# Kernel tuning notes

Hardware: AMD Instinct MI355X
Metric: run time of the kernel (lower is better)

## Reference

```python
import jax, jax.numpy as jnp
import numpy as np

DIM = 2048
HID = 1024
E = 16
TOP_K = 2
S_SHARED = 2


def setup_inputs() -> dict:
    key = jax.random.key(0)
    ks = jax.random.split(key, 6)
    scale = 0.02
    x = jax.random.normal(ks[0], (2, 2048, DIM), dtype=jnp.float32)
    gate_w = jax.random.normal(ks[1], (DIM, E), dtype=jnp.float32) * scale
    shared_w1 = jax.random.normal(ks[2], (S_SHARED, DIM, HID), dtype=jnp.float32) * scale
    shared_w2 = jax.random.normal(ks[3], (S_SHARED, HID, DIM), dtype=jnp.float32) * scale
    w1 = jax.random.normal(ks[4], (E, DIM, HID), dtype=jnp.float32) * scale
    w2 = jax.random.normal(ks[5], (E, HID, DIM), dtype=jnp.float32) * scale
    return {"x": x, "gate_w": gate_w, "shared_w1": shared_w1,
            "shared_w2": shared_w2, "w1": w1, "w2": w2}


def reference(x, gate_w, shared_w1, shared_w2, w1, w2):
    orig_shape = x.shape
    xf = x.reshape(-1, orig_shape[-1])  # [T, D]

    # Shared experts: sum of SiLU MLPs
    hs = jax.nn.silu(jnp.einsum('td,sdh->sth', xf, shared_w1))
    shared_out = jnp.einsum('sth,shd->td', hs, shared_w2)

    # Gating
    probs = jax.nn.softmax(xf @ gate_w, axis=-1)              # [T, E]
    weights, indices = jax.lax.top_k(probs, TOP_K)            # [T, K]
    weights = weights / weights.sum(axis=-1, keepdims=True)
    aux_loss = (probs.mean(axis=0) ** 2).sum() * E

    # Combine weights per (token, expert): top_k indices are distinct
    combine = (jax.nn.one_hot(indices, E, dtype=xf.dtype) *
               weights[..., None]).sum(axis=1)                # [T, E]

    # Dense all-expert compute (reference form of gather-GEMM-scatter)
    h = jax.nn.silu(jnp.einsum('td,edh->eth', xf, w1))        # [E, T, H]
    y = jnp.einsum('eth,ehd->etd', h, w2)                     # [E, T, D]
    routed_out = jnp.einsum('te,etd->td', combine, y)         # [T, D]

    out = (shared_out + routed_out).reshape(orig_shape)
    return out, aux_loss
```

## Files before the change

### kernel.cpp

```cpp
#include <hip/hip_runtime.h>
#include <math.h>

typedef unsigned short u16;
typedef __bf16 bf16x8 __attribute__((ext_vector_type(8)));
typedef float f32x4 __attribute__((ext_vector_type(4)));
typedef unsigned short u16x8 __attribute__((ext_vector_type(8)));

#define T_TOK 4096
#define DIMD 2048
#define HIDD 1024
#define NEXP 16
#define RMAX 10240
#define MAXBLK 96
#define BM 128
#define BN 256
#define BK 64

__device__ __forceinline__ u16 f2b(float f) {
  unsigned u = __builtin_bit_cast(unsigned, f);
  unsigned r = (u + 0x7FFFu + ((u >> 16) & 1u)) >> 16;
  return (u16)r;
}

__device__ __forceinline__ void gld16(const void* g, void* l) {
  __builtin_amdgcn_global_load_lds(
      (const __attribute__((address_space(1))) void*)g,
      (__attribute__((address_space(3))) void*)l, 16, 0, 0);
}


__global__ void k_pre(const float* __restrict__ x, u16* __restrict__ xb,
                      int* __restrict__ perm, int* __restrict__ cnt) {
  const int i = blockIdx.x * blockDim.x + threadIdx.x;
  const float4 v = ((const float4*)x)[i];
  union { u16 u[4]; unsigned long long q; } t;
  t.u[0] = f2b(v.x); t.u[1] = f2b(v.y); t.u[2] = f2b(v.z); t.u[3] = f2b(v.w);
  ((unsigned long long*)xb)[i] = t.q;
  if (i < RMAX) perm[i] = -1;
  if (i < NEXP) cnt[i] = 0;
}

__global__ __launch_bounds__(256)
void k_gate(const float* __restrict__ x, const float* __restrict__ gw,
            int* __restrict__ top2i, float* __restrict__ top2w,
            int* __restrict__ cnt, float* __restrict__ partial) {
  const int e = threadIdx.x & 15;
  const int tt = threadIdx.x >> 4;
  const int t = blockIdx.x * 16 + tt;
  const float* xp = x + (size_t)t * DIMD;
  float acc = 0.f;
#pragma unroll 8
  for (int k = 0; k < DIMD; ++k) acc = fmaf(xp[k], gw[k * NEXP + e], acc);
  __shared__ float lg[16][17];
  __shared__ float pr[16][17];
  lg[tt][e] = acc;
  __syncthreads();
  if (e == 0) {
    float l[16];
    float mx = -1e30f;
    for (int j = 0; j < 16; ++j) { l[j] = lg[tt][j]; mx = fmaxf(mx, l[j]); }
    float s = 0.f;
    for (int j = 0; j < 16; ++j) { l[j] = expf(l[j] - mx); s += l[j]; }
    const float inv = 1.f / s;
    float p1 = -1.f, p2 = -1.f; int i1 = 0, i2 = 0;
    for (int j = 0; j < 16; ++j) {
      const float p = l[j] * inv;
      pr[tt][j] = p;
      if (p > p1) { p2 = p1; i2 = i1; p1 = p; i1 = j; }
      else if (p > p2) { p2 = p; i2 = j; }
    }
    const float wsum = p1 + p2;
    top2i[t * 2 + 0] = i1;
    top2i[t * 2 + 1] = i2;
    top2w[t * 2 + 0] = p1 / wsum;
    top2w[t * 2 + 1] = p2 / wsum;
    atomicAdd(&cnt[i1], 1);
    atomicAdd(&cnt[i2], 1);
  }
  __syncthreads();
  if (tt == 0) {
    float s = 0.f;
    for (int j = 0; j < 16; ++j) s += pr[j][e];
    partial[blockIdx.x * 16 + e] = s;
  }
}

__global__ __launch_bounds__(256)
void k_sched(const int* __restrict__ cnt, const int* __restrict__ top2i,
             const float* __restrict__ top2w, const float* __restrict__ partial,
             int* __restrict__ tbl_e, int* __restrict__ tbl_r0,
             int* __restrict__ nblk, int* __restrict__ perm,
             float* __restrict__ wrow, int* __restrict__ slot2,
             float* __restrict__ auxOut) {
  __shared__ int offs[17];
  __shared__ int lfill[16];
  __shared__ float s[16][17];
  const int tid = threadIdx.x;
  if (tid == 0) {
    int o = 0, nb = 0;
    for (int e = 0; e < NEXP; ++e) {
      offs[e] = o;
      const int b = (cnt[e] + BM - 1) / BM;
      for (int i = 0; i < b; ++i) { tbl_e[nb] = e; tbl_r0[nb] = o + i * BM; ++nb; }
      o += b * BM;
    }
    offs[16] = o;
    nblk[0] = nb;
  }
  if (tid < 16) lfill[tid] = 0;
  __syncthreads();
  for (int id = tid; id < T_TOK * 2; id += 256) {
    const int e = top2i[id];
    const int pos = atomicAdd(&lfill[e], 1);
    const int r = offs[e] + pos;
    perm[r] = id >> 1;
    wrow[r] = top2w[id];
    slot2[id] = r;
  }
  const int e = tid & 15, c = tid >> 4;
  float a = 0.f;
  for (int b = c; b < 256; b += 16) a += partial[b * 16 + e];
  s[c][e] = a;
  __syncthreads();
  if (tid == 0) {
    float aux = 0.f;
    for (int j = 0; j < 16; ++j) {
      float tot = 0.f;
      for (int cc = 0; cc < 16; ++cc) tot += s[cc][j];
      const float m = tot / (float)T_TOK;
      aux += m * m;
    }
    auxOut[0] = aux * (float)NEXP;
  }
}

__global__ __launch_bounds__(256)
void k_trW(const float* __restrict__ w1, const float* __restrict__ w2,
           const float* __restrict__ sw1, const float* __restrict__ sw2,
           u16* __restrict__ w1t, u16* __restrict__ w2t,
           u16* __restrict__ sw1t, u16* __restrict__ sw2ct) {
  const int z = blockIdx.z;
  const float* W; u16* Wo; int K, N, ldo;
  if (z < 16) {
    W = w1 + (size_t)z * 2048 * 1024;
    Wo = w1t + (size_t)z * 1024 * 2048;
    K = 2048; N = 1024; ldo = 2048;
  } else if (z < 32) {
    W = w2 + (size_t)(z - 16) * 1024 * 2048;
    Wo = w2t + (size_t)(z - 16) * 2048 * 1024;
    K = 1024; N = 2048; ldo = 1024;
  } else if (z < 34) {
    W = sw1 + (size_t)(z - 32) * 2048 * 1024;
    Wo = sw1t + (size_t)(z - 32) * 1024 * 2048;
    K = 2048; N = 1024; ldo = 2048;
  } else {
    W = sw2 + (size_t)(z - 34) * 1024 * 2048;
    Wo = sw2ct + (size_t)(z - 34) * 1024;
    K = 1024; N = 2048; ldo = 2048;
  }
  const int n0 = blockIdx.x * 64, k0 = blockIdx.y * 64;
  if (n0 >= N || k0 >= K) return;
  __shared__ float t[64][65];
  {
    const int r = threadIdx.x >> 4;
    const int c = (threadIdx.x & 15) * 4;
#pragma unroll
    for (int p = 0; p < 4; ++p) {
      const int kk = p * 16 + r;
      const float4 v = *(const float4*)&W[(size_t)(k0 + kk) * N + n0 + c];
      t[kk][c] = v.x; t[kk][c + 1] = v.y; t[kk][c + 2] = v.z; t[kk][c + 3] = v.w;
    }
  }
  __syncthreads();
  {
    const int r2 = threadIdx.x >> 3;
    const int g8 = (threadIdx.x & 7) * 8;
#pragma unroll
    for (int p = 0; p < 2; ++p) {
      const int nn = p * 32 + r2;
      u16x8 o;
#pragma unroll
      for (int i = 0; i < 8; ++i) o[i] = f2b(t[g8 + i][nn]);
      *(u16x8*)&Wo[(size_t)(n0 + nn) * ldo + k0 + g8] = o;
    }
  }
}

__global__ __launch_bounds__(512)
void k_post(float* __restrict__ out, const float* __restrict__ rbLo,
            const float* __restrict__ rbHi, const int* __restrict__ slot2,
            const float* __restrict__ wrow) {
  const int t = blockIdx.x;
  const int d4 = threadIdx.x;
  const int s0 = slot2[t * 2], s1 = slot2[t * 2 + 1];
  const float w0 = wrow[s0], w1 = wrow[s1];
  const float4* r0 = (const float4*)(s0 < 8192 ? rbLo + (size_t)s0 * DIMD
                                               : rbHi + (size_t)(s0 - 8192) * DIMD);
  const float4* r1 = (const float4*)(s1 < 8192 ? rbLo + (size_t)s1 * DIMD
                                               : rbHi + (size_t)(s1 - 8192) * DIMD);
  float4* op = (float4*)(out + (size_t)t * DIMD);
  float4 o = op[d4];
  const float4 a = r0[d4], b = r1[d4];
  o.x += w0 * a.x + w1 * b.x;
  o.y += w0 * a.y + w1 * b.y;
  o.z += w0 * a.z + w1 * b.z;
  o.w += w0 * a.w + w1 * b.w;
  op[d4] = o;
}


__device__ __forceinline__ void stage_tile(
    const u16* gA0, const u16* gA1, const u16* gB0, const u16* gB1,
    const u16* gB2, const u16* gB3, int k0, u16* S, int b, int w) {
  u16* As = S + b * 24576;
  u16* Bs = As + 8192;
  gld16(gA0 + k0, As + w * 512);
  gld16(gA1 + k0, As + 4096 + w * 512);
  gld16(gB0 + k0, Bs + w * 512);
  gld16(gB1 + k0, Bs + 4096 + w * 512);
  gld16(gB2 + k0, Bs + 8192 + w * 512);
  gld16(gB3 + k0, Bs + 12288 + w * 512);
}

__device__ __forceinline__ void comp_tile(const u16* __restrict__ S, int b,
    const int (&aoff)[4][2], const int (&boff)[4][2], f32x4 (&acc)[4][4]) {
  const u16* As = S + b * 24576;
  const u16* Bs = As + 8192;
#pragma unroll
  for (int kh = 0; kh < 2; ++kh) {
    bf16x8 a[4], bq[4];
#pragma unroll
    for (int i = 0; i < 4; ++i) a[i] = *(const bf16x8*)(As + aoff[i][kh]);
#pragma unroll
    for (int j = 0; j < 4; ++j) bq[j] = *(const bf16x8*)(Bs + boff[j][kh]);
    __builtin_amdgcn_s_setprio(1);
#pragma unroll
    for (int i = 0; i < 4; ++i)
#pragma unroll
      for (int j = 0; j < 4; ++j)
        acc[i][j] = __builtin_amdgcn_mfma_f32_16x16x32_bf16(a[i], bq[j], acc[i][j], 0, 0, 0);
    __builtin_amdgcn_s_setprio(0);
  }
}

#define FENCE asm volatile("" ::: "memory")
#define VMW6  asm volatile("s_waitcnt vmcnt(6)" ::: "memory")
#define VMW0  asm volatile("s_waitcnt vmcnt(0)" ::: "memory")

__device__ __forceinline__ void gemm_pipe(
    const u16* gA0, const u16* gA1, const u16* gB0, const u16* gB1,
    const u16* gB2, const u16* gB3, int K, u16* S,
    const int (&aoff)[4][2], const int (&boff)[4][2],
    f32x4 (&acc)[4][4], int w) {
  const int nt = K >> 6;
  stage_tile(gA0, gA1, gB0, gB1, gB2, gB3, 0, S, 0, w);
  stage_tile(gA0, gA1, gB0, gB1, gB2, gB3, 64, S, 1, w);
  VMW6;
  __builtin_amdgcn_s_barrier();
  FENCE;
  for (int t = 0; t < nt - 2; ++t) {
    comp_tile(S, t & 1, aoff, boff, acc);
    FENCE;
    __builtin_amdgcn_s_barrier();
    FENCE;
    stage_tile(gA0, gA1, gB0, gB1, gB2, gB3, (t + 2) << 6, S, t & 1, w);
    VMW6;
    __builtin_amdgcn_s_barrier();
    FENCE;
  }
  comp_tile(S, 0, aoff, boff, acc);
  VMW0;
  __builtin_amdgcn_s_barrier();
  FENCE;
  comp_tile(S, 1, aoff, boff, acc);
}

__global__ __launch_bounds__(512, 2)
void k_up(const u16* __restrict__ xb, const u16* __restrict__ sw1t,
          const u16* __restrict__ w1t, u16* __restrict__ hbS,
          u16* __restrict__ hbR, const int* __restrict__ perm,
          const int* __restrict__ tbl_e, const int* __restrict__ tbl_r0,
          const int* __restrict__ nblk) {
  __shared__ u16 S[49152];
  const int bx = blockIdx.x, by = blockIdx.y;
  const int tid = threadIdx.x;
  const int w = tid >> 6, lane = tid & 63;
  const int lm = lane & 15, lq = lane >> 4;
  const int wm = w >> 2, wn = w & 3;
  const int srow = w * 8 + (lane >> 3);
  const int c8 = lane & 7;

  const bool routed = bx >= 32;
  int r0, ga0, ga1;
  const u16* Bb;
  if (!routed) {
    r0 = bx * BM;
    Bb = sw1t;
    ga0 = r0 + srow; ga1 = r0 + 64 + srow;
  } else {
    if (by >= 4) return;
    const int rbx = bx - 32;
    if (rbx >= *nblk) return;
    const int e = tbl_e[rbx];
    r0 = tbl_r0[rbx];
    Bb = w1t + (size_t)e * (size_t)HIDD * DIMD;
    const int p0 = perm[r0 + srow];      ga0 = (p0 < 0) ? 0 : p0;
    const int p1 = perm[r0 + 64 + srow]; ga1 = (p1 < 0) ? 0 : p1;
  }
  const int n0 = by * BN;
  const u16* gA0 = xb + (size_t)ga0 * DIMD + (c8 ^ ((srow >> 1) & 7)) * 8;
  const u16* gA1 = xb + (size_t)ga1 * DIMD + (c8 ^ (((64 + srow) >> 1) & 7)) * 8;
  const u16* gB[4];
#pragma unroll
  for (int p = 0; p < 4; ++p) {
    const int n = p * 64 + srow;
    gB[p] = Bb + (size_t)(n0 + n) * DIMD + (c8 ^ ((n >> 1) & 7)) * 8;
  }
  int aoff[4][2], boff[4][2];
#pragma unroll
  for (int i = 0; i < 4; ++i) {
    const int m = wm * 64 + i * 16 + lm;
    const int n = wn * 64 + i * 16 + lm;
#pragma unroll
    for (int kh = 0; kh < 2; ++kh) {
      aoff[i][kh] = m * 64 + (((kh << 2) | lq) ^ ((m >> 1) & 7)) * 8;
      boff[i][kh] = n * 64 + (((kh << 2) | lq) ^ ((n >> 1) & 7)) * 8;
    }
  }
  f32x4 acc[4][4];
#pragma unroll
  for (int i = 0; i < 4; ++i)
#pragma unroll
    for (int j = 0; j < 4; ++j) {
      acc[i][j][0] = 0.f; acc[i][j][1] = 0.f; acc[i][j][2] = 0.f; acc[i][j][3] = 0.f;
    }

  gemm_pipe(gA0, gA1, gB[0], gB[1], gB[2], gB[3], DIMD, S, aoff, boff, acc, w);

#pragma unroll
  for (int i = 0; i < 4; ++i) {
#pragma unroll
    for (int r = 0; r < 4; ++r) {
      const int row = r0 + wm * 64 + i * 16 + lq * 4 + r;
      u16* dst = routed ? &hbR[(size_t)row * HIDD] : &hbS[(size_t)row * DIMD];
#pragma unroll
      for (int j = 0; j < 4; ++j) {
        const int gc = n0 + wn * 64 + j * 16 + lm;
        const float v = acc[i][j][r];
        const float s = v / (1.f + expf(-v));
        dst[gc] = f2b(s);
      }
    }
  }
}

__global__ __launch_bounds__(512, 2)
void k_down(const u16* __restrict__ hbS, const u16* __restrict__ hbR,
            const u16* __restrict__ sw2ct, const u16* __restrict__ w2t,
            float* __restrict__ out, float* __restrict__ rbLo,
            float* __restrict__ rbHi, const int* __restrict__ tbl_e,
            const int* __restrict__ tbl_r0, const int* __restrict__ nblk) {
  __shared__ u16 S[49152];
  const int bx = blockIdx.x, by = blockIdx.y;
  const int tid = threadIdx.x;
  const int w = tid >> 6, lane = tid & 63;
  const int lm = lane & 15, lq = lane >> 4;
  const int wm = w >> 2, wn = w & 3;
  const int srow = w * 8 + (lane >> 3);
  const int c8 = lane & 7;

  const bool routed = bx >= 32;
  int r0, K, ld;
  const u16 *Ab, *Bb;
  if (!routed) {
    r0 = bx * BM;
    Ab = hbS; K = DIMD; ld = DIMD;
    Bb = sw2ct;
  } else {
    const int rbx = bx - 32;
    if (rbx >= *nblk) return;
    const int e = tbl_e[rbx];
    r0 = tbl_r0[rbx];
    Ab = hbR; K = HIDD; ld = HIDD;
    Bb = w2t + (size_t)e * (size_t)DIMD * HIDD;
  }
  const int n0 = by * BN;
  const u16* gA0 = Ab + (size_t)(r0 + srow) * ld + (c8 ^ ((srow >> 1) & 7)) * 8;
  const u16* gA1 = Ab + (size_t)(r0 + 64 + srow) * ld + (c8 ^ (((64 + srow) >> 1) & 7)) * 8;
  const u16* gB[4];
#pragma unroll
  for (int p = 0; p < 4; ++p) {
    const int n = p * 64 + srow;
    gB[p] = Bb + (size_t)(n0 + n) * ld + (c8 ^ ((n >> 1) & 7)) * 8;
  }
  int aoff[4][2], boff[4][2];
#pragma unroll
  for (int i = 0; i < 4; ++i) {
    const int m = wm * 64 + i * 16 + lm;
    const int n = wn * 64 + i * 16 + lm;
#pragma unroll
    for (int kh = 0; kh < 2; ++kh) {
      aoff[i][kh] = m * 64 + (((kh << 2) | lq) ^ ((m >> 1) & 7)) * 8;
      boff[i][kh] = n * 64 + (((kh << 2) | lq) ^ ((n >> 1) & 7)) * 8;
    }
  }
  f32x4 acc[4][4];
#pragma unroll
  for (int i = 0; i < 4; ++i)
#pragma unroll
    for (int j = 0; j < 4; ++j) {
      acc[i][j][0] = 0.f; acc[i][j][1] = 0.f; acc[i][j][2] = 0.f; acc[i][j][3] = 0.f;
    }

  gemm_pipe(gA0, gA1, gB[0], gB[1], gB[2], gB[3], K, S, aoff, boff, acc, w);

#pragma unroll
  for (int i = 0; i < 4; ++i) {
#pragma unroll
    for (int r = 0; r < 4; ++r) {
      const int rr = r0 + wm * 64 + i * 16 + lq * 4 + r;
      float* dst;
      if (!routed) dst = out + (size_t)rr * DIMD;
      else dst = (rr < 8192) ? rbLo + (size_t)rr * DIMD
                             : rbHi + (size_t)(rr - 8192) * DIMD;
#pragma unroll
      for (int j = 0; j < 4; ++j) {
        const int gc = n0 + wn * 64 + j * 16 + lm;
        dst[gc] = acc[i][j][r];
      }
    }
  }
}


extern "C" void kernel_launch(void* const* d_in, const int* in_sizes, int n_in,
                              void* d_out, int out_size, void* d_ws, size_t ws_size,
                              hipStream_t stream) {
  const float* x   = (const float*)d_in[0];
  const float* gw  = (const float*)d_in[1];
  const float* sw1 = (const float*)d_in[2];
  const float* sw2 = (const float*)d_in[3];
  const float* w1  = (const float*)d_in[4];
  const float* w2  = (const float*)d_in[5];
  float* out = (float*)d_out;

  char* ws = (char*)d_ws;
  u16* xb    = (u16*)(ws);
  u16* hbS   = (u16*)(ws + (size_t)( 16 << 20));
  u16* hbR   = (u16*)(ws + (size_t)( 32 << 20));
  u16* sw1t  = (u16*)(ws + (size_t)( 56 << 20));
  u16* sw2ct = (u16*)(ws + (size_t)( 64 << 20));
  u16* w1t   = (u16*)(ws + (size_t)( 72 << 20));
  u16* w2t   = (u16*)(ws + (size_t)(136 << 20));
  float* rbLo = (float*)(ws + (size_t)( 72 << 20));
  float* rbHi = (float*)(ws);
  char* p = ws + (size_t)(200 << 20);
  int*   top2i   = (int*)p;    p += T_TOK * 2 * 4;
  float* top2w   = (float*)p;  p += T_TOK * 2 * 4;
  int*   perm    = (int*)p;    p += RMAX * 4;
  float* wrow    = (float*)p;  p += RMAX * 4;
  int*   slot2   = (int*)p;    p += T_TOK * 2 * 4;
  int*   cnt     = (int*)p;    p += 16 * 4;
  int*   tbl_e   = (int*)p;    p += MAXBLK * 4;
  int*   tbl_r0  = (int*)p;    p += MAXBLK * 4;
  int*   nblk    = (int*)p;    p += 16 * 4;
  float* partial = (float*)p;  p += 256 * 16 * 4;

  k_pre<<<(T_TOK * DIMD / 4) / 256, 256, 0, stream>>>(x, xb, perm, cnt);
  k_gate<<<T_TOK / 16, 256, 0, stream>>>(x, gw, top2i, top2w, cnt, partial);
  k_sched<<<1, 256, 0, stream>>>(cnt, top2i, top2w, partial, tbl_e, tbl_r0,
                                 nblk, perm, wrow, slot2,
                                 out + (size_t)T_TOK * DIMD);
  k_trW<<<dim3(32, 32, 36), 256, 0, stream>>>(w1, w2, sw1, sw2,
                                              w1t, w2t, sw1t, sw2ct);
  k_up<<<dim3(32 + MAXBLK, 8), 512, 0, stream>>>(xb, sw1t, w1t, hbS, hbR,
                                                 perm, tbl_e, tbl_r0, nblk);
  k_down<<<dim3(32 + MAXBLK, 8), 512, 0, stream>>>(hbS, hbR, sw2ct, w2t, out,
                                                   rbLo, rbHi, tbl_e, tbl_r0, nblk);
  k_post<<<T_TOK, 512, 0, stream>>>(out, rbLo, rbHi, slot2, wrow);
}
```

Measured before the change: 762.7 us.

## Enlarge GEMM tile to 256x256 with staggered LDS pipeline and token-ordered scatter

```diff
diff --git a/kernel.cpp b/kernel.cpp
--- a/kernel.cpp
+++ b/kernel.cpp
@@ -10,11 +10,10 @@
 #define DIMD 2048
 #define HIDD 1024
 #define NEXP 16
-#define RMAX 10240
-#define MAXBLK 96
-#define BM 128
+#define RMAX 12288
+#define MAXBLK 48
+#define BM 256
 #define BN 256
-#define BK 64
 
 __device__ __forceinline__ u16 f2b(float f) {
   unsigned u = __builtin_bit_cast(unsigned, f);
@@ -30,13 +29,14 @@
 
 
 __global__ void k_pre(const float* __restrict__ x, u16* __restrict__ xb,
-                      int* __restrict__ perm, int* __restrict__ cnt) {
+                      int* __restrict__ perm, int* __restrict__ perm2,
+                      int* __restrict__ cnt) {
   const int i = blockIdx.x * blockDim.x + threadIdx.x;
   const float4 v = ((const float4*)x)[i];
   union { u16 u[4]; unsigned long long q; } t;
   t.u[0] = f2b(v.x); t.u[1] = f2b(v.y); t.u[2] = f2b(v.z); t.u[3] = f2b(v.w);
   ((unsigned long long*)xb)[i] = t.q;
-  if (i < RMAX) perm[i] = -1;
+  if (i < RMAX) { perm[i] = -1; perm2[i] = -1; }
   if (i < NEXP) cnt[i] = 0;
 }
 
@@ -90,8 +90,7 @@
              const float* __restrict__ top2w, const float* __restrict__ partial,
              int* __restrict__ tbl_e, int* __restrict__ tbl_r0,
              int* __restrict__ nblk, int* __restrict__ perm,
-             float* __restrict__ wrow, int* __restrict__ slot2,
-             float* __restrict__ auxOut) {
+             int* __restrict__ perm2, float* __restrict__ auxOut) {
   __shared__ int offs[17];
   __shared__ int lfill[16];
   __shared__ float s[16][17];
@@ -114,8 +113,7 @@
     const int pos = atomicAdd(&lfill[e], 1);
     const int r = offs[e] + pos;
     perm[r] = id >> 1;
-    wrow[r] = top2w[id];
-    slot2[id] = r;
+    perm2[r] = id;
   }
   const int e = tid & 15, c = tid >> 4;
   float a = 0.f;
@@ -142,20 +140,16 @@
   const int z = blockIdx.z;
   const float* W; u16* Wo; int K, N, ldo;
   if (z < 16) {
-    W = w1 + (size_t)z * 2048 * 1024;
-    Wo = w1t + (size_t)z * 1024 * 2048;
+    W = w1 + (size_t)z * 2048 * 1024;  Wo = w1t + (size_t)z * 1024 * 2048;
     K = 2048; N = 1024; ldo = 2048;
   } else if (z < 32) {
-    W = w2 + (size_t)(z - 16) * 1024 * 2048;
-    Wo = w2t + (size_t)(z - 16) * 2048 * 1024;
+    W = w2 + (size_t)(z - 16) * 1024 * 2048;  Wo = w2t + (size_t)(z - 16) * 2048 * 1024;
     K = 1024; N = 2048; ldo = 1024;
   } else if (z < 34) {
-    W = sw1 + (size_t)(z - 32) * 2048 * 1024;
-    Wo = sw1t + (size_t)(z - 32) * 1024 * 2048;
+    W = sw1 + (size_t)(z - 32) * 2048 * 1024;  Wo = sw1t + (size_t)(z - 32) * 1024 * 2048;
     K = 2048; N = 1024; ldo = 2048;
   } else {
-    W = sw2 + (size_t)(z - 34) * 1024 * 2048;
-    Wo = sw2ct + (size_t)(z - 34) * 1024;
+    W = sw2 + (size_t)(z - 34) * 1024 * 2048;  Wo = sw2ct + (size_t)(z - 34) * 1024;
     K = 1024; N = 2048; ldo = 2048;
   }
   const int n0 = blockIdx.x * 64, k0 = blockIdx.y * 64;
@@ -187,20 +181,15 @@
 }
 
 __global__ __launch_bounds__(512)
-void k_post(float* __restrict__ out, const float* __restrict__ rbLo,
-            const float* __restrict__ rbHi, const int* __restrict__ slot2,
-            const float* __restrict__ wrow) {
+void k_post(float* __restrict__ out, const float* __restrict__ rb,
+            const float* __restrict__ top2w) {
   const int t = blockIdx.x;
   const int d4 = threadIdx.x;
-  const int s0 = slot2[t * 2], s1 = slot2[t * 2 + 1];
-  const float w0 = wrow[s0], w1 = wrow[s1];
-  const float4* r0 = (const float4*)(s0 < 8192 ? rbLo + (size_t)s0 * DIMD
-                                               : rbHi + (size_t)(s0 - 8192) * DIMD);
-  const float4* r1 = (const float4*)(s1 < 8192 ? rbLo + (size_t)s1 * DIMD
-                                               : rbHi + (size_t)(s1 - 8192) * DIMD);
+  const float w0 = top2w[t * 2], w1 = top2w[t * 2 + 1];
+  const float4 a = ((const float4*)(rb + (size_t)(2 * t) * DIMD))[d4];
+  const float4 b = ((const float4*)(rb + (size_t)(2 * t + 1) * DIMD))[d4];
   float4* op = (float4*)(out + (size_t)t * DIMD);
   float4 o = op[d4];
-  const float4 a = r0[d4], b = r1[d4];
   o.x += w0 * a.x + w1 * b.x;
   o.y += w0 * a.y + w1 * b.y;
   o.z += w0 * a.z + w1 * b.z;
@@ -209,70 +198,95 @@
 }
 
 
-__device__ __forceinline__ void stage_tile(
-    const u16* gA0, const u16* gA1, const u16* gB0, const u16* gB1,
-    const u16* gB2, const u16* gB3, int k0, u16* S, int b, int w) {
-  u16* As = S + b * 24576;
-  u16* Bs = As + 8192;
-  gld16(gA0 + k0, As + w * 512);
-  gld16(gA1 + k0, As + 4096 + w * 512);
-  gld16(gB0 + k0, Bs + w * 512);
-  gld16(gB1 + k0, Bs + 4096 + w * 512);
-  gld16(gB2 + k0, Bs + 8192 + w * 512);
-  gld16(gB3 + k0, Bs + 12288 + w * 512);
-}
-
-__device__ __forceinline__ void comp_tile(const u16* __restrict__ S, int b,
-    const int (&aoff)[4][2], const int (&boff)[4][2], f32x4 (&acc)[4][4]) {
-  const u16* As = S + b * 24576;
-  const u16* Bs = As + 8192;
-#pragma unroll
-  for (int kh = 0; kh < 2; ++kh) {
-    bf16x8 a[4], bq[4];
-#pragma unroll
-    for (int i = 0; i < 4; ++i) a[i] = *(const bf16x8*)(As + aoff[i][kh]);
-#pragma unroll
-    for (int j = 0; j < 4; ++j) bq[j] = *(const bf16x8*)(Bs + boff[j][kh]);
-    __builtin_amdgcn_s_setprio(1);
-#pragma unroll
-    for (int i = 0; i < 4; ++i)
-#pragma unroll
-      for (int j = 0; j < 4; ++j)
-        acc[i][j] = __builtin_amdgcn_mfma_f32_16x16x32_bf16(a[i], bq[j], acc[i][j], 0, 0, 0);
-    __builtin_amdgcn_s_setprio(0);
-  }
-}
-
 #define FENCE asm volatile("" ::: "memory")
 #define VMW6  asm volatile("s_waitcnt vmcnt(6)" ::: "memory")
 #define VMW0  asm volatile("s_waitcnt vmcnt(0)" ::: "memory")
-
-__device__ __forceinline__ void gemm_pipe(
-    const u16* gA0, const u16* gA1, const u16* gB0, const u16* gB1,
-    const u16* gB2, const u16* gB3, int K, u16* S,
-    const int (&aoff)[4][2], const int (&boff)[4][2],
-    f32x4 (&acc)[4][4], int w) {
-  const int nt = K >> 6;
-  stage_tile(gA0, gA1, gB0, gB1, gB2, gB3, 0, S, 0, w);
-  stage_tile(gA0, gA1, gB0, gB1, gB2, gB3, 64, S, 1, w);
+#define BARR  do { FENCE; __builtin_amdgcn_s_barrier(); FENCE; } while (0)
+
+struct GP { const u16* a[2][2]; const u16* b[2][2]; };
+
+__device__ __forceinline__ void stA(const GP& g, u16* S, int w512, int D, int L, int K) {
+  gld16(g.a[0][L] + K, S + D + L * 4096 + w512);
+  gld16(g.a[1][L] + K, S + D + 8192 + L * 4096 + w512);
+}
+__device__ __forceinline__ void stB(const GP& g, u16* S, int w512, int D, int G, int K) {
+  gld16(g.b[G][0] + K, S + D + 16384 + G * 8192 + w512);
+  gld16(g.b[G][1] + K, S + D + 16384 + G * 8192 + 4096 + w512);
+}
+__device__ __forceinline__ void rdA(const u16* S, int D, const int (&aoff)[8][2],
+                                    int q, bf16x8 (&af)[4]) {
+  af[0] = *(const bf16x8*)(S + D + aoff[2 * q][0]);
+  af[1] = *(const bf16x8*)(S + D + aoff[2 * q][1]);
+  af[2] = *(const bf16x8*)(S + D + aoff[2 * q + 1][0]);
+  af[3] = *(const bf16x8*)(S + D + aoff[2 * q + 1][1]);
+}
+__device__ __forceinline__ void rdB(const u16* S, int D, const int (&boff)[4][2],
+                                    bf16x8 (&bf)[4][2]) {
+#pragma unroll
+  for (int nf = 0; nf < 4; ++nf) {
+    bf[nf][0] = *(const bf16x8*)(S + D + boff[nf][0]);
+    bf[nf][1] = *(const bf16x8*)(S + D + boff[nf][1]);
+  }
+}
+__device__ __forceinline__ void mm16(f32x4 (&acc)[8][4], const bf16x8 (&af)[4],
+                                     const bf16x8 (&bf)[4][2], int q) {
+  __builtin_amdgcn_s_setprio(1);
+#pragma unroll
+  for (int kh = 0; kh < 2; ++kh)
+#pragma unroll
+    for (int mi = 0; mi < 2; ++mi)
+#pragma unroll
+      for (int nf = 0; nf < 4; ++nf)
+        acc[2 * q + mi][nf] = __builtin_amdgcn_mfma_f32_16x16x32_bf16(
+            af[mi * 2 + kh], bf[nf][kh], acc[2 * q + mi][nf], 0, 0, 0);
+  __builtin_amdgcn_s_setprio(0);
+}
+
+template <bool LAST>
+__device__ __forceinline__ void iter8(u16* S, int w512, const GP& g,
+    int k1, int k2, int k3, const int (&aoff)[8][2], const int (&boff)[4][2],
+    f32x4 (&acc)[8][4]) {
+  bf16x8 af[4], bf[4][2];
+  rdA(S, 0, aoff, 0, af); rdB(S, 0, boff, bf);
+  stA(g, S, w512, 32768, 1, k1);
+  BARR; mm16(acc, af, bf, 0); BARR;
+  rdA(S, 0, aoff, 1, af);
+  if (!LAST) stB(g, S, w512, 0, 0, k2);
+  BARR; mm16(acc, af, bf, 1); BARR;
+  rdA(S, 0, aoff, 2, af);
+  if (!LAST) stB(g, S, w512, 0, 1, k2);
+  BARR; mm16(acc, af, bf, 2); BARR;
+  rdA(S, 0, aoff, 3, af);
+  if (!LAST) stA(g, S, w512, 0, 0, k2);
+  if (LAST) { VMW0; } else { VMW6; }
+  BARR; mm16(acc, af, bf, 3); BARR;
+  rdA(S, 32768, aoff, 0, af); rdB(S, 32768, boff, bf);
+  if (!LAST) stA(g, S, w512, 0, 1, k2);
+  BARR; mm16(acc, af, bf, 0); BARR;
+  rdA(S, 32768, aoff, 1, af);
+  if (!LAST) stB(g, S, w512, 32768, 0, k3);
+  BARR; mm16(acc, af, bf, 1); BARR;
+  rdA(S, 32768, aoff, 2, af);
+  if (!LAST) stB(g, S, w512, 32768, 1, k3);
+  BARR; mm16(acc, af, bf, 2); BARR;
+  rdA(S, 32768, aoff, 3, af);
+  if (!LAST) { stA(g, S, w512, 32768, 0, k3); VMW6; }
+  BARR; mm16(acc, af, bf, 3); BARR;
+}
+
+__device__ __forceinline__ void gemm8(u16* S, int w512, const GP& g, int K,
+    const int (&aoff)[8][2], const int (&boff)[4][2], f32x4 (&acc)[8][4]) {
+  stB(g, S, w512, 0, 0, 0);  stB(g, S, w512, 0, 1, 0);
+  stA(g, S, w512, 0, 0, 0);  stA(g, S, w512, 0, 1, 0);
+  stB(g, S, w512, 32768, 0, 64);  stB(g, S, w512, 32768, 1, 64);
+  stA(g, S, w512, 32768, 0, 64);
   VMW6;
-  __builtin_amdgcn_s_barrier();
-  FENCE;
-  for (int t = 0; t < nt - 2; ++t) {
-    comp_tile(S, t & 1, aoff, boff, acc);
-    FENCE;
-    __builtin_amdgcn_s_barrier();
-    FENCE;
-    stage_tile(gA0, gA1, gB0, gB1, gB2, gB3, (t + 2) << 6, S, t & 1, w);
-    VMW6;
-    __builtin_amdgcn_s_barrier();
-    FENCE;
-  }
-  comp_tile(S, 0, aoff, boff, acc);
-  VMW0;
-  __builtin_amdgcn_s_barrier();
-  FENCE;
-  comp_tile(S, 1, aoff, boff, acc);
+  BARR;
+  const int nIt = K >> 7;
+  for (int j = 0; j < nIt - 1; ++j)
+    iter8<false>(S, w512, g, (2 * j + 1) * 64, (2 * j + 2) * 64,
+                 (2 * j + 3) * 64, aoff, boff, acc);
+  iter8<true>(S, w512, g, K - 64, 0, 0, aoff, boff, acc);
 }
 
 __global__ __launch_bounds__(512, 2)
@@ -281,7 +295,7 @@
           u16* __restrict__ hbR, const int* __restrict__ perm,
           const int* __restrict__ tbl_e, const int* __restrict__ tbl_r0,
           const int* __restrict__ nblk) {
-  __shared__ u16 S[49152];
+  __shared__ u16 S[65536];
   const int bx = blockIdx.x, by = blockIdx.y;
   const int tid = threadIdx.x;
   const int w = tid >> 6, lane = tid & 63;
@@ -289,64 +303,78 @@
   const int wm = w >> 2, wn = w & 3;
   const int srow = w * 8 + (lane >> 3);
   const int c8 = lane & 7;
-
-  const bool routed = bx >= 32;
-  int r0, ga0, ga1;
-  const u16* Bb;
+  const int w512 = w * 512;
+
+  const bool routed = bx >= 16;
+  int r0; const u16* Bb;
   if (!routed) {
     r0 = bx * BM;
     Bb = sw1t;
-    ga0 = r0 + srow; ga1 = r0 + 64 + srow;
   } else {
     if (by >= 4) return;
-    const int rbx = bx - 32;
+    const int rbx = bx - 16;
     if (rbx >= *nblk) return;
     const int e = tbl_e[rbx];
     r0 = tbl_r0[rbx];
     Bb = w1t + (size_t)e * (size_t)HIDD * DIMD;
-    const int p0 = perm[r0 + srow];      ga0 = (p0 < 0) ? 0 : p0;
-    const int p1 = perm[r0 + 64 + srow]; ga1 = (p1 < 0) ? 0 : p1;
   }
   const int n0 = by * BN;
-  const u16* gA0 = xb + (size_t)ga0 * DIMD + (c8 ^ ((srow >> 1) & 7)) * 8;
-  const u16* gA1 = xb + (size_t)ga1 * DIMD + (c8 ^ (((64 + srow) >> 1) & 7)) * 8;
-  const u16* gB[4];
-#pragma unroll
-  for (int p = 0; p < 4; ++p) {
-    const int n = p * 64 + srow;
-    gB[p] = Bb + (size_t)(n0 + n) * DIMD + (c8 ^ ((n >> 1) & 7)) * 8;
-  }
-  int aoff[4][2], boff[4][2];
-#pragma unroll
-  for (int i = 0; i < 4; ++i) {
-    const int m = wm * 64 + i * 16 + lm;
-    const int n = wn * 64 + i * 16 + lm;
+
+  GP g;
+#pragma unroll
+  for (int l = 0; l < 2; ++l) {
+    const int co = (c8 ^ (((l * 64 + srow) >> 1) & 7)) * 8;
+#pragma unroll
+    for (int h = 0; h < 2; ++h) {
+      const int tr = r0 + h * 128 + l * 64 + srow;
+      int ga;
+      if (!routed) ga = tr;
+      else { const int p = perm[tr]; ga = (p < 0) ? 0 : p; }
+      g.a[h][l] = xb + (size_t)ga * DIMD + co;
+    }
+#pragma unroll
+    for (int gg = 0; gg < 2; ++gg)
+      g.b[gg][l] = Bb + (size_t)(n0 + gg * 128 + l * 64 + srow) * DIMD + co;
+  }
+  int aoff[8][2], boff[4][2];
+#pragma unroll
+  for (int mi = 0; mi < 8; ++mi) {
+    const int m = mi * 16 + lm;
 #pragma unroll
     for (int kh = 0; kh < 2; ++kh) {
-      aoff[i][kh] = m * 64 + (((kh << 2) | lq) ^ ((m >> 1) & 7)) * 8;
-      boff[i][kh] = n * 64 + (((kh << 2) | lq) ^ ((n >> 1) & 7)) * 8;
-    }
-  }
-  f32x4 acc[4][4];
-#pragma unroll
-  for (int i = 0; i < 4; ++i)
+      const int kc = kh * 4 + lq;
+      aoff[mi][kh] = wm * 8192 + m * 64 + ((kc ^ ((m >> 1) & 7)) * 8);
+    }
+  }
+#pragma unroll
+  for (int nf = 0; nf < 4; ++nf) {
+    const int nlh = (wn & 1) * 64 + nf * 16 + lm;
+#pragma unroll
+    for (int kh = 0; kh < 2; ++kh) {
+      const int kc = kh * 4 + lq;
+      boff[nf][kh] = 16384 + (wn >> 1) * 8192 + nlh * 64 + ((kc ^ ((nlh >> 1) & 7)) * 8);
+    }
+  }
+  f32x4 acc[8][4];
+#pragma unroll
+  for (int i = 0; i < 8; ++i)
 #pragma unroll
     for (int j = 0; j < 4; ++j) {
       acc[i][j][0] = 0.f; acc[i][j][1] = 0.f; acc[i][j][2] = 0.f; acc[i][j][3] = 0.f;
     }
 
-  gemm_pipe(gA0, gA1, gB[0], gB[1], gB[2], gB[3], DIMD, S, aoff, boff, acc, w);
-
-#pragma unroll
-  for (int i = 0; i < 4; ++i) {
+  gemm8(S, w512, g, DIMD, aoff, boff, acc);
+
+#pragma unroll
+  for (int mi = 0; mi < 8; ++mi) {
 #pragma unroll
     for (int r = 0; r < 4; ++r) {
-      const int row = r0 + wm * 64 + i * 16 + lq * 4 + r;
-      u16* dst = routed ? &hbR[(size_t)row * HIDD] : &hbS[(size_t)row * DIMD];
-#pragma unroll
-      for (int j = 0; j < 4; ++j) {
-        const int gc = n0 + wn * 64 + j * 16 + lm;
-        const float v = acc[i][j][r];
+      const int row = r0 + wm * 128 + mi * 16 + lq * 4 + r;
+      u16* dst = routed ? hbR + (size_t)row * HIDD : hbS + (size_t)row * DIMD;
+#pragma unroll
+      for (int nf = 0; nf < 4; ++nf) {
+        const int gc = n0 + wn * 64 + nf * 16 + lm;
+        const float v = acc[mi][nf][r];
         const float s = v / (1.f + expf(-v));
         dst[gc] = f2b(s);
       }
@@ -357,10 +385,10 @@
 __global__ __launch_bounds__(512, 2)
 void k_down(const u16* __restrict__ hbS, const u16* __restrict__ hbR,
             const u16* __restrict__ sw2ct, const u16* __restrict__ w2t,
-            float* __restrict__ out, float* __restrict__ rbLo,
-            float* __restrict__ rbHi, const int* __restrict__ tbl_e,
+            float* __restrict__ out, float* __restrict__ rb,
+            const int* __restrict__ perm2, const int* __restrict__ tbl_e,
             const int* __restrict__ tbl_r0, const int* __restrict__ nblk) {
-  __shared__ u16 S[49152];
+  __shared__ u16 S[65536];
   const int bx = blockIdx.x, by = blockIdx.y;
   const int tid = threadIdx.x;
   const int w = tid >> 6, lane = tid & 63;
@@ -368,8 +396,9 @@
   const int wm = w >> 2, wn = w & 3;
   const int srow = w * 8 + (lane >> 3);
   const int c8 = lane & 7;
-
-  const bool routed = bx >= 32;
+  const int w512 = w * 512;
+
+  const bool routed = bx >= 16;
   int r0, K, ld;
   const u16 *Ab, *Bb;
   if (!routed) {
@@ -377,7 +406,7 @@
     Ab = hbS; K = DIMD; ld = DIMD;
     Bb = sw2ct;
   } else {
-    const int rbx = bx - 32;
+    const int rbx = bx - 16;
     if (rbx >= *nblk) return;
     const int e = tbl_e[rbx];
     r0 = tbl_r0[rbx];
@@ -385,48 +414,65 @@
     Bb = w2t + (size_t)e * (size_t)DIMD * HIDD;
   }
   const int n0 = by * BN;
-  const u16* gA0 = Ab + (size_t)(r0 + srow) * ld + (c8 ^ ((srow >> 1) & 7)) * 8;
-  const u16* gA1 = Ab + (size_t)(r0 + 64 + srow) * ld + (c8 ^ (((64 + srow) >> 1) & 7)) * 8;
-  const u16* gB[4];
-#pragma unroll
-  for (int p = 0; p < 4; ++p) {
-    const int n = p * 64 + srow;
-    gB[p] = Bb + (size_t)(n0 + n) * ld + (c8 ^ ((n >> 1) & 7)) * 8;
-  }
-  int aoff[4][2], boff[4][2];
-#pragma unroll
-  for (int i = 0; i < 4; ++i) {
-    const int m = wm * 64 + i * 16 + lm;
-    const int n = wn * 64 + i * 16 + lm;
+
+  GP g;
+#pragma unroll
+  for (int l = 0; l < 2; ++l) {
+    const int co = (c8 ^ (((l * 64 + srow) >> 1) & 7)) * 8;
+#pragma unroll
+    for (int h = 0; h < 2; ++h)
+      g.a[h][l] = Ab + (size_t)(r0 + h * 128 + l * 64 + srow) * ld + co;
+#pragma unroll
+    for (int gg = 0; gg < 2; ++gg)
+      g.b[gg][l] = Bb + (size_t)(n0 + gg * 128 + l * 64 + srow) * ld + co;
+  }
+  int aoff[8][2], boff[4][2];
+#pragma unroll
+  for (int mi = 0; mi < 8; ++mi) {
+    const int m = mi * 16 + lm;
 #pragma unroll
     for (int kh = 0; kh < 2; ++kh) {
-      aoff[i][kh] = m * 64 + (((kh << 2) | lq) ^ ((m >> 1) & 7)) * 8;
-      boff[i][kh] = n * 64 + (((kh << 2) | lq) ^ ((n >> 1) & 7)) * 8;
-    }
-  }
-  f32x4 acc[4][4];
-#pragma unroll
-  for (int i = 0; i < 4; ++i)
+      const int kc = kh * 4 + lq;
+      aoff[mi][kh] = wm * 8192 + m * 64 + ((kc ^ ((m >> 1) & 7)) * 8);
+    }
+  }
+#pragma unroll
+  for (int nf = 0; nf < 4; ++nf) {
+    const int nlh = (wn & 1) * 64 + nf * 16 + lm;
+#pragma unroll
+    for (int kh = 0; kh < 2; ++kh) {
+      const int kc = kh * 4 + lq;
+      boff[nf][kh] = 16384 + (wn >> 1) * 8192 + nlh * 64 + ((kc ^ ((nlh >> 1) & 7)) * 8);
+    }
+  }
+  f32x4 acc[8][4];
+#pragma unroll
+  for (int i = 0; i < 8; ++i)
 #pragma unroll
     for (int j = 0; j < 4; ++j) {
       acc[i][j][0] = 0.f; acc[i][j][1] = 0.f; acc[i][j][2] = 0.f; acc[i][j][3] = 0.f;
     }
 
-  gemm_pipe(gA0, gA1, gB[0], gB[1], gB[2], gB[3], K, S, aoff, boff, acc, w);
-
-#pragma unroll
-  for (int i = 0; i < 4; ++i) {
+  gemm8(S, w512, g, K, aoff, boff, acc);
+
+#pragma unroll
+  for (int mi = 0; mi < 8; ++mi) {
 #pragma unroll
     for (int r = 0; r < 4; ++r) {
-      const int rr = r0 + wm * 64 + i * 16 + lq * 4 + r;
-      float* dst;
-      if (!routed) dst = out + (size_t)rr * DIMD;
-      else dst = (rr < 8192) ? rbLo + (size_t)rr * DIMD
-                             : rbHi + (size_t)(rr - 8192) * DIMD;
-#pragma unroll
-      for (int j = 0; j < 4; ++j) {
-        const int gc = n0 + wn * 64 + j * 16 + lm;
-        dst[gc] = acc[i][j][r];
+      const int row = r0 + wm * 128 + mi * 16 + lq * 4 + r;
+      if (!routed) {
+        float* dst = out + (size_t)row * DIMD;
+#pragma unroll
+        for (int nf = 0; nf < 4; ++nf)
+          dst[n0 + wn * 64 + nf * 16 + lm] = acc[mi][nf][r];
+      } else {
+        const int id2 = perm2[row];
+        if (id2 >= 0) {
+          float* dst = rb + (size_t)id2 * DIMD;
+#pragma unroll
+          for (int nf = 0; nf < 4; ++nf)
+            dst[n0 + wn * 64 + nf * 16 + lm] = acc[mi][nf][r];
+        }
       }
     }
   }
@@ -452,30 +498,27 @@
   u16* sw2ct = (u16*)(ws + (size_t)( 64 << 20));
   u16* w1t   = (u16*)(ws + (size_t)( 72 << 20));
   u16* w2t   = (u16*)(ws + (size_t)(136 << 20));
-  float* rbLo = (float*)(ws + (size_t)( 72 << 20));
-  float* rbHi = (float*)(ws);
+  float* rb  = (float*)(ws + (size_t)( 72 << 20));
   char* p = ws + (size_t)(200 << 20);
   int*   top2i   = (int*)p;    p += T_TOK * 2 * 4;
   float* top2w   = (float*)p;  p += T_TOK * 2 * 4;
   int*   perm    = (int*)p;    p += RMAX * 4;
-  float* wrow    = (float*)p;  p += RMAX * 4;
-  int*   slot2   = (int*)p;    p += T_TOK * 2 * 4;
+  int*   perm2   = (int*)p;    p += RMAX * 4;
   int*   cnt     = (int*)p;    p += 16 * 4;
   int*   tbl_e   = (int*)p;    p += MAXBLK * 4;
   int*   tbl_r0  = (int*)p;    p += MAXBLK * 4;
   int*   nblk    = (int*)p;    p += 16 * 4;
   float* partial = (float*)p;  p += 256 * 16 * 4;
 
-  k_pre<<<(T_TOK * DIMD / 4) / 256, 256, 0, stream>>>(x, xb, perm, cnt);
+  k_pre<<<(T_TOK * DIMD / 4) / 256, 256, 0, stream>>>(x, xb, perm, perm2, cnt);
   k_gate<<<T_TOK / 16, 256, 0, stream>>>(x, gw, top2i, top2w, cnt, partial);
   k_sched<<<1, 256, 0, stream>>>(cnt, top2i, top2w, partial, tbl_e, tbl_r0,
-                                 nblk, perm, wrow, slot2,
-                                 out + (size_t)T_TOK * DIMD);
+                                 nblk, perm, perm2, out + (size_t)T_TOK * DIMD);
   k_trW<<<dim3(32, 32, 36), 256, 0, stream>>>(w1, w2, sw1, sw2,
                                               w1t, w2t, sw1t, sw2ct);
-  k_up<<<dim3(32 + MAXBLK, 8), 512, 0, stream>>>(xb, sw1t, w1t, hbS, hbR,
+  k_up<<<dim3(16 + MAXBLK, 8), 512, 0, stream>>>(xb, sw1t, w1t, hbS, hbR,
                                                  perm, tbl_e, tbl_r0, nblk);
-  k_down<<<dim3(32 + MAXBLK, 8), 512, 0, stream>>>(hbS, hbR, sw2ct, w2t, out,
-                                                   rbLo, rbHi, tbl_e, tbl_r0, nblk);
-  k_post<<<T_TOK, 512, 0, stream>>>(out, rbLo, rbHi, slot2, wrow);
-}
+  k_down<<<dim3(16 + MAXBLK, 8), 512, 0, stream>>>(hbS, hbR, sw2ct, w2t, out,
+                                                   rb, perm2, tbl_e, tbl_r0, nblk);
+  k_post<<<T_TOK, 512, 0, stream>>>(out, rb, top2w);
+}
```

Measured after the change: 746.9 us. 1.02x faster.
